# Performance work log

Hardware: AMD Instinct MI355X
Metric: run time of the kernel (lower is better)

## Reference

```python
import jax, jax.numpy as jnp
import numpy as np

DIM = 256      # channel dim
NW = 7         # n_win per side
HEADS = 8
TOPK = 4
KVW = 4        # kv_per_win (ada_avgpool output side)
EPS = 1e-6


def _dwconv(x, w, b):
    # depthwise conv, NHWC, 'SAME' == padding k//2 for odd kernels
    y = jax.lax.conv_general_dilated(
        x, w, (1, 1), 'SAME',
        dimension_numbers=('NHWC', 'HWIO', 'NHWC'),
        feature_group_count=x.shape[-1])
    return y + b


def _ln(x, g, b):
    mu = x.mean(-1, keepdims=True)
    var = ((x - mu) ** 2).mean(-1, keepdims=True)
    return (x - mu) * jax.lax.rsqrt(var + EPS) * g + b


def _bra(x, qkv_w, qkv_b, wo_w, wo_b, lepe_w, lepe_b):
    # BiLevelRoutingAttention, x: (n, H, W, C)
    n, H, W, C = x.shape
    hw, ww = H // NW, W // NW          # window size (8, 8)
    scale = C ** -0.5                   # qk_dim ** -0.5 (BiFormer uses full qk_dim)
    qkv = x @ qkv_w.T + qkv_b           # (n, H, W, 3C)
    # window partition: n (j hw) (i ww) c -> n (j i) hw ww c
    qkv_win = qkv.reshape(n, NW, hw, NW, ww, 3 * C)
    qkv_win = qkv_win.transpose(0, 1, 3, 2, 4, 5).reshape(n, NW * NW, hw, ww, 3 * C)
    q = qkv_win[..., :C]                # (n, p2, hw, ww, C)
    kv = qkv_win[..., C:]               # (n, p2, hw, ww, 2C)
    # --- window-level routing (q/k detached in torch; no fwd effect) ---
    q_win = q.mean((2, 3))              # (n, p2, C)
    k_win = kv[..., :C].mean((2, 3))    # (n, p2, C)
    logits = jnp.einsum('npc,nqc->npq', q_win * scale, k_win)
    _, idx = jax.lax.top_k(logits, TOPK)            # (n, p2, k)
    # --- kv downsample: adaptive avg pool (hw,ww)->(KVW,KVW), exact 2x2 mean here ---
    fh, fw = hw // KVW, ww // KVW
    kv_pix = kv.reshape(n, NW * NW, KVW, fh, KVW, fw, 2 * C).mean((3, 5))
    kv_pix = kv_pix.reshape(n, NW * NW, KVW * KVW, 2 * C)   # (n, p2, w2, 2C)
    # --- gather top-k windows' kv ---
    kv_sel = jax.vmap(lambda t, ix: t[ix])(kv_pix, idx)     # (n, p2, k, w2, 2C)
    cph = C // HEADS
    k_sel = kv_sel[..., :C].reshape(n, NW * NW, TOPK * KVW * KVW, HEADS, cph)
    v_sel = kv_sel[..., C:].reshape(n, NW * NW, TOPK * KVW * KVW, HEADS, cph)
    q_pix = q.reshape(n, NW * NW, hw * ww, HEADS, cph)
    # --- windowed attention over gathered tokens ---
    att = jnp.einsum('npqmc,npsmc->npmqs', q_pix * scale, k_sel)
    att = jax.nn.softmax(att, axis=-1)
    out = jnp.einsum('npmqs,npsmc->npqmc', att, v_sel)
    out = out.reshape(n, NW, NW, hw, ww, C).transpose(0, 1, 3, 2, 4, 5).reshape(n, H, W, C)
    # --- lepe: depthwise 5x5 on v over the full image ---
    v_img = qkv[..., 2 * C:]
    out = out + _dwconv(v_img, lepe_w, lepe_b)
    return out @ wo_w.T + wo_b


def setup_inputs() -> dict:
    key = jax.random.key(0)
    ks = jax.random.split(key, 8)
    C, s = DIM, 0.02
    p = {}
    p['x'] = jax.random.normal(ks[0], (16, C, 56, 56), jnp.float32)
    p['pos_w'] = jax.random.normal(ks[1], (3, 3, 1, C), jnp.float32) * s
    p['pos_b'] = jnp.zeros((C,), jnp.float32)
    p['ln1_g'] = jnp.ones((C,), jnp.float32)
    p['ln1_b'] = jnp.zeros((C,), jnp.float32)
    p['ln2_g'] = jnp.ones((C,), jnp.float32)
    p['ln2_b'] = jnp.zeros((C,), jnp.float32)
    p['qkv_w'] = jax.random.normal(ks[2], (3 * C, C), jnp.float32) * s
    p['qkv_b'] = jnp.zeros((3 * C,), jnp.float32)
    p['wo_w'] = jax.random.normal(ks[3], (C, C), jnp.float32) * s
    p['wo_b'] = jnp.zeros((C,), jnp.float32)
    p['lepe_w'] = jax.random.normal(ks[4], (5, 5, 1, C), jnp.float32) * s
    p['lepe_b'] = jnp.zeros((C,), jnp.float32)
    p['fc1_w'] = jax.random.normal(ks[5], (4 * C, C), jnp.float32) * s
    p['fc1_b'] = jnp.zeros((4 * C,), jnp.float32)
    p['fc2_w'] = jax.random.normal(ks[6], (C, 4 * C), jnp.float32) * s
    p['fc2_b'] = jnp.zeros((C,), jnp.float32)
    return p


def reference(x, pos_w, pos_b, ln1_g, ln1_b, ln2_g, ln2_b, qkv_w, qkv_b,
              wo_w, wo_b, lepe_w, lepe_b, fc1_w, fc1_b, fc2_w, fc2_b):
    xh = x.transpose(0, 2, 3, 1)                       # NCHW -> NHWC
    xh = xh + _dwconv(xh, pos_w, pos_b)                # pos embed (dw 3x3)
    xh = xh + _bra(_ln(xh, ln1_g, ln1_b), qkv_w, qkv_b, wo_w, wo_b, lepe_w, lepe_b)
    h = _ln(xh, ln2_g, ln2_b)
    h = jax.nn.gelu(h @ fc1_w.T + fc1_b, approximate=False)
    xh = xh + (h @ fc2_w.T + fc2_b)
    return xh.transpose(0, 3, 1, 2)                    # NHWC -> NCHW
```

## Files before the change

kernel.cpp:

```cpp
#include <hip/hip_runtime.h>
#include <math.h>

static constexpr int NIMG = 16;
static constexpr int TOK  = NIMG * 56 * 56;
static constexpr size_t TC = (size_t)TOK * 256;
static constexpr int PTOK = 784 * 16;

typedef __bf16 bf16x8 __attribute__((ext_vector_type(8)));
typedef float  f32x4  __attribute__((ext_vector_type(4)));

__device__ inline float bf2f(unsigned short u) {
  unsigned int i = ((unsigned int)u) << 16; float f; __builtin_memcpy(&f, &i, 4); return f;
}
__device__ inline unsigned short f2bf(float f) {
  unsigned int i; __builtin_memcpy(&i, &f, 4);
  unsigned int r = i + 0x7fffu + ((i >> 16) & 1u);
  return (unsigned short)(r >> 16);
}

__global__ __launch_bounds__(256) void nchw2nhwc(const float* __restrict__ x,
                                                 float* __restrict__ y) {
  __shared__ float tile[32][33];
  int nh = blockIdx.z;
  int n = nh / 56, h = nh % 56;
  int c0 = blockIdx.y * 32, w0 = blockIdx.x * 32;
  int tx = threadIdx.x, ty = threadIdx.y;
#pragma unroll
  for (int i = 0; i < 4; i++) {
    int c = c0 + ty + i * 8, w = w0 + tx;
    if (w < 56) tile[ty + i * 8][tx] = x[(((size_t)n * 256 + c) * 56 + h) * 56 + w];
  }
  __syncthreads();
#pragma unroll
  for (int i = 0; i < 4; i++) {
    int w = w0 + ty + i * 8, c = c0 + tx;
    if (w < 56) y[(((size_t)n * 56 + h) * 56 + w) * 256 + c] = tile[tx][ty + i * 8];
  }
}

__global__ __launch_bounds__(256) void nhwc2nchw(const float* __restrict__ y,
                                                 float* __restrict__ o) {
  __shared__ float tile[32][33];
  int nh = blockIdx.z;
  int n = nh / 56, h = nh % 56;
  int w0 = blockIdx.x * 32, c0 = blockIdx.y * 32;
  int tx = threadIdx.x, ty = threadIdx.y;
#pragma unroll
  for (int i = 0; i < 4; i++) {
    int w = w0 + ty + i * 8, c = c0 + tx;
    if (w < 56) tile[ty + i * 8][tx] = y[(((size_t)n * 56 + h) * 56 + w) * 256 + c];
  }
  __syncthreads();
#pragma unroll
  for (int i = 0; i < 4; i++) {
    int c = c0 + ty + i * 8, w = w0 + tx;
    if (w < 56) o[(((size_t)n * 256 + c) * 56 + h) * 56 + w] = tile[tx][ty + i * 8];
  }
}

__global__ __launch_bounds__(256) void posconv_kernel(const float* __restrict__ xt,
                                                      const float* __restrict__ w,
                                                      const float* __restrict__ b,
                                                      float* __restrict__ xh) {
  int t = blockIdx.x * 4 + (threadIdx.x >> 6);
  int lane = threadIdx.x & 63;
  int c = lane * 4;
  int n = t / 3136, rem = t % 3136, h = rem / 56, ww = rem % 56;
  f32x4 acc = *(const f32x4*)&b[c];
  for (int dh = -1; dh <= 1; dh++) {
    int hh = h + dh;
    if ((unsigned)hh >= 56u) continue;
    for (int dw = -1; dw <= 1; dw++) {
      int wc = ww + dw;
      if ((unsigned)wc >= 56u) continue;
      f32x4 xx = *(const f32x4*)&xt[(((size_t)n * 56 + hh) * 56 + wc) * 256 + c];
      f32x4 wv = *(const f32x4*)&w[((dh + 1) * 3 + (dw + 1)) * 256 + c];
      acc += xx * wv;
    }
  }
  f32x4 xv = *(const f32x4*)&xt[(size_t)t * 256 + c];
  *(f32x4*)&xh[(size_t)t * 256 + c] = xv + acc;
}

__global__ __launch_bounds__(256) void lnw_kernel(const float* __restrict__ x,
                                                  const float* __restrict__ g,
                                                  const float* __restrict__ b,
                                                  float* __restrict__ of,
                                                  unsigned short* __restrict__ ob) {
  int t = blockIdx.x * 4 + (threadIdx.x >> 6);
  int lane = threadIdx.x & 63;
  int c = lane * 4;
  f32x4 v = *(const f32x4*)&x[(size_t)t * 256 + c];
  float s = v[0] + v[1] + v[2] + v[3];
#pragma unroll
  for (int m = 1; m < 64; m <<= 1) s += __shfl_xor(s, m);
  float mu = s * (1.f / 256.f);
  f32x4 d = v - mu;
  float ss = d[0] * d[0] + d[1] * d[1] + d[2] * d[2] + d[3] * d[3];
#pragma unroll
  for (int m = 1; m < 64; m <<= 1) ss += __shfl_xor(ss, m);
  float rs = rsqrtf(ss * (1.f / 256.f) + 1e-6f);
  f32x4 gg = *(const f32x4*)&g[c];
  f32x4 bb = *(const f32x4*)&b[c];
  f32x4 y = d * rs * gg + bb;
  if (of) *(f32x4*)&of[(size_t)t * 256 + c] = y;
  if (ob) {
    unsigned short yb[4];
#pragma unroll
    for (int j = 0; j < 4; j++) yb[j] = f2bf(y[j]);
    __builtin_memcpy(ob + (size_t)t * 256 + c, yb, 8);
  }
}

template <bool OUTBF, bool LN2F>
__global__ __launch_bounds__(512, 4) void mgemm2(const unsigned short* __restrict__ A, int lda,
                                                 const unsigned short* __restrict__ B, int ldb,
                                                 const float* __restrict__ bias,
                                                 const float* __restrict__ R,
                                                 void* __restrict__ C_,
                                                 int N, int K, int flags, int gx,
                                                 const float* __restrict__ g2,
                                                 const float* __restrict__ b2,
                                                 unsigned short* __restrict__ ob2) {
  __shared__ unsigned short As[128 * 64];
  __shared__ unsigned short Bs[256 * 64];
  __shared__ float redS[4][128];
  __shared__ float redQ[4][128];
  int tid = threadIdx.x;
  int nwg = gridDim.x, bid = blockIdx.x;
  int q8 = nwg >> 3, r8 = nwg & 7;
  int xcd = bid & 7, pos = bid >> 3;
  int wgid = (xcd < r8 ? xcd * (q8 + 1) : r8 * (q8 + 1) + (xcd - r8) * q8) + pos;
  int m0 = (wgid / gx) * 128;
  int n0 = (wgid % gx) * 256;

  int lane = tid & 63, wid = tid >> 6;
  int wr = (wid >> 2) * 64, wc = (wid & 3) * 64;
  int llo = lane & 15, lhi = lane >> 4;

  f32x4 acc[4][4];
#pragma unroll
  for (int i = 0; i < 4; i++)
#pragma unroll
    for (int j = 0; j < 4; j++) acc[i][j] = (f32x4){0.f, 0.f, 0.f, 0.f};

  for (int k0 = 0; k0 < K; k0 += 64) {
#pragma unroll
    for (int i = 0; i < 2; i++) {
      int qa = tid + 512 * i;
      int row = qa >> 3, col = (qa & 7) ^ (row & 7);
      __builtin_amdgcn_global_load_lds(
          (const __attribute__((address_space(1))) unsigned int*)
              (A + (size_t)(m0 + row) * lda + k0 + col * 8),
          (__attribute__((address_space(3))) unsigned int*)(As + qa * 8), 16, 0, 0);
    }
#pragma unroll
    for (int i = 0; i < 4; i++) {
      int qb = tid + 512 * i;
      int row = qb >> 3, col = (qb & 7) ^ (row & 7);
      __builtin_amdgcn_global_load_lds(
          (const __attribute__((address_space(1))) unsigned int*)
              (B + (size_t)(n0 + row) * ldb + k0 + col * 8),
          (__attribute__((address_space(3))) unsigned int*)(Bs + qb * 8), 16, 0, 0);
    }
    __syncthreads();
#pragma unroll
    for (int ks = 0; ks < 2; ks++) {
      int cchunk = ks * 4 + lhi;
      bf16x8 af[4], bfr[4];
#pragma unroll
      for (int mi = 0; mi < 4; mi++) {
        int r = wr + mi * 16 + llo;
        __builtin_memcpy(&af[mi], As + (size_t)r * 64 + (cchunk ^ (r & 7)) * 8, 16);
      }
#pragma unroll
      for (int nj = 0; nj < 4; nj++) {
        int r = wc + nj * 16 + llo;
        __builtin_memcpy(&bfr[nj], Bs + (size_t)r * 64 + (cchunk ^ (r & 7)) * 8, 16);
      }
#pragma unroll
      for (int mi = 0; mi < 4; mi++)
#pragma unroll
        for (int nj = 0; nj < 4; nj++)
          acc[mi][nj] = __builtin_amdgcn_mfma_f32_16x16x32_bf16(af[mi], bfr[nj],
                                                                acc[mi][nj], 0, 0, 0);
    }
    __syncthreads();
  }

  if constexpr (LN2F) {
    float sr[4][4], qr[4][4];
#pragma unroll
    for (int mi = 0; mi < 4; mi++)
#pragma unroll
      for (int j = 0; j < 4; j++) { sr[mi][j] = 0.f; qr[mi][j] = 0.f; }
#pragma unroll
    for (int mi = 0; mi < 4; mi++)
#pragma unroll
      for (int nj = 0; nj < 4; nj++) {
        int n = wc + nj * 16 + llo;
        float bv = bias[n];
#pragma unroll
        for (int j = 0; j < 4; j++) {
          int m = m0 + wr + mi * 16 + lhi * 4 + j;
          float v = acc[mi][nj][j] + bv + R[(size_t)m * 256 + n];
          acc[mi][nj][j] = v;
          sr[mi][j] += v;
          qr[mi][j] += v * v;
        }
      }
#pragma unroll
    for (int mi = 0; mi < 4; mi++)
#pragma unroll
      for (int j = 0; j < 4; j++)
#pragma unroll
        for (int d = 1; d < 16; d <<= 1) {
          sr[mi][j] += __shfl_xor(sr[mi][j], d);
          qr[mi][j] += __shfl_xor(qr[mi][j], d);
        }
    if (llo == 0) {
#pragma unroll
      for (int mi = 0; mi < 4; mi++)
#pragma unroll
        for (int j = 0; j < 4; j++) {
          int lr = wr + mi * 16 + lhi * 4 + j;
          redS[wid & 3][lr] = sr[mi][j];
          redQ[wid & 3][lr] = qr[mi][j];
        }
    }
    __syncthreads();
#pragma unroll
    for (int mi = 0; mi < 4; mi++)
#pragma unroll
      for (int j = 0; j < 4; j++) {
        int lr = wr + mi * 16 + lhi * 4 + j;
        float S = redS[0][lr] + redS[1][lr] + redS[2][lr] + redS[3][lr];
        float Q = redQ[0][lr] + redQ[1][lr] + redQ[2][lr] + redQ[3][lr];
        float mu = S * (1.f / 256.f);
        float var = Q * (1.f / 256.f) - mu * mu;
        float rs = rsqrtf(var + 1e-6f);
        size_t mrow = (size_t)(m0 + lr) * 256;
#pragma unroll
        for (int nj = 0; nj < 4; nj++) {
          int n = wc + nj * 16 + llo;
          float v = acc[mi][nj][j];
          ((float*)C_)[mrow + n] = v;
          ob2[mrow + n] = f2bf((v - mu) * rs * g2[n] + b2[n]);
        }
      }
  } else {
    int coln = llo, rowg = lhi * 4;
#pragma unroll
    for (int mi = 0; mi < 4; mi++) {
#pragma unroll
      for (int nj = 0; nj < 4; nj++) {
        int n = n0 + wc + nj * 16 + coln;
        float bv = (flags & 8) ? 0.f : bias[n];
#pragma unroll
        for (int j = 0; j < 4; j++) {
          int m = m0 + wr + mi * 16 + rowg + j;
          float v = acc[mi][nj][j] + bv;
          if (flags & 1) v = 0.5f * v * (1.0f + erff(v * 0.70710678118654752f));
          if (flags & 2) v += R[(size_t)m * N + n];
          if (OUTBF) ((unsigned short*)C_)[(size_t)m * N + n] = f2bf(v);
          else       ((float*)C_)[(size_t)m * N + n] = v;
        }
      }
    }
  }
}

__global__ __launch_bounds__(256) void cvt_kernel(const float* __restrict__ s,
                                                  unsigned short* __restrict__ d, int n) {
  int i = blockIdx.x * 256 + threadIdx.x;
  if (i < n) d[i] = f2bf(s[i]);
}

__global__ __launch_bounds__(512) void bqv_kernel(const float* __restrict__ qkv_b,
                                                  float* __restrict__ bqv) {
  int i = threadIdx.x;
  bqv[i] = qkv_b[i < 256 ? i : i + 256];
}

__global__ __launch_bounds__(256) void pool_kernel(const float* __restrict__ x,
                                                   unsigned short* __restrict__ plx,
                                                   float* __restrict__ wmx) {
  int np = blockIdx.x, c = threadIdx.x;
  int n = np / 49, p = np % 49, wr = p / 7, wc = p % 7;
  float tot = 0.f;
  for (int s = 0; s < 16; s++) {
    int i = s >> 2, j = s & 3;
    float a = 0.f;
    for (int di = 0; di < 2; di++)
      for (int dj = 0; dj < 2; dj++) {
        size_t t = ((size_t)n * 56 + wr * 8 + i * 2 + di) * 56 + wc * 8 + j * 2 + dj;
        a += x[t * 256 + c];
      }
    a *= 0.25f;
    plx[((size_t)np * 16 + s) * 256 + c] = f2bf(a);
    tot += a;
  }
  wmx[(size_t)np * 256 + c] = tot * (1.f / 16.f);
}

__global__ __launch_bounds__(256) void winproj_kernel(const float* __restrict__ wmx,
                                                      const float* __restrict__ qkv_w,
                                                      const float* __restrict__ qkv_b,
                                                      float* __restrict__ qkwin) {
  int np = blockIdx.x, t = threadIdx.x;
  __shared__ float xs[256];
  xs[t] = wmx[(size_t)np * 256 + t];
  __syncthreads();
  for (int rep = 0; rep < 2; rep++) {
    int n = t + rep * 256;
    const float* wrow = qkv_w + (size_t)n * 256;
    float s = qkv_b[n];
    for (int c = 0; c < 256; c++) s += xs[c] * wrow[c];
    qkwin[(size_t)np * 512 + n] = s;
  }
}

__global__ __launch_bounds__(64) void topk_kernel(const float* __restrict__ qkwin,
                                                  int* __restrict__ idx) {
  int np = blockIdx.x;
  int n = np / 49;
  int j = threadIdx.x;
  __shared__ float lg[49];
  if (j < 49) {
    const float* qp = qkwin + (size_t)np * 512;
    const float* kp = qkwin + ((size_t)n * 49 + j) * 512 + 256;
    float s = 0.f;
    for (int c = 0; c < 256; c++) s += qp[c] * kp[c];
    lg[j] = s;
  }
  __syncthreads();
  if (j == 0) {
    unsigned long long used = 0ull;
    for (int t = 0; t < 4; t++) {
      float best = -INFINITY;
      int bi = 0;
      for (int q = 0; q < 49; q++)
        if (!((used >> q) & 1ull) && lg[q] > best) { best = lg[q]; bi = q; }
      idx[np * 4 + t] = bi;
      used |= (1ull << bi);
    }
  }
}

__global__ __launch_bounds__(64) void attn_mfma(const unsigned short* __restrict__ qvb,
                                                const unsigned short* __restrict__ kvp,
                                                const int* __restrict__ idx,
                                                unsigned short* __restrict__ out) {
  __shared__ unsigned short Vt[32 * 72];
  __shared__ unsigned short Pl[64 * 72];
  int bid = blockIdx.x;
  int head = bid & 7, np = bid >> 3;
  int n = np / 49, p = np % 49;
  int h0 = (p / 7) * 8, w0 = (p % 7) * 8;
  int lane = threadIdx.x;
  int lhi = lane >> 4, llo = lane & 15;

  int wi4[4];
#pragma unroll
  for (int t = 0; t < 4; t++) wi4[t] = idx[np * 4 + t];

#pragma unroll
  for (int it = 0; it < 4; it++) {
    int cell = lane >> 2;
    int chunk = lane & 3;
    int s = it * 16 + cell;
    const unsigned short* g = kvp + ((size_t)(n * 49 + wi4[it]) * 16 + cell) * 512
                              + 256 + head * 32 + chunk * 8;
    unsigned short vv[8];
    __builtin_memcpy(vv, g, 16);
#pragma unroll
    for (int j = 0; j < 8; j++) Vt[(chunk * 8 + j) * 72 + s] = vv[j];
  }

  bf16x8 qf[4], kf[4];
#pragma unroll
  for (int mi = 0; mi < 4; mi++) {
    int row = mi * 16 + llo;
    int h = h0 + (row >> 3), w = w0 + (row & 7);
    __builtin_memcpy(&qf[mi],
                     qvb + (((size_t)n * 56 + h) * 56 + w) * 512 + head * 32 + lhi * 8, 16);
  }
#pragma unroll
  for (int nj = 0; nj < 4; nj++) {
    __builtin_memcpy(&kf[nj],
                     kvp + ((size_t)(n * 49 + wi4[nj]) * 16 + llo) * 512 + head * 32 + lhi * 8,
                     16);
  }

  f32x4 acc[4][4];
#pragma unroll
  for (int mi = 0; mi < 4; mi++)
#pragma unroll
    for (int nj = 0; nj < 4; nj++) acc[mi][nj] = (f32x4){0.f, 0.f, 0.f, 0.f};
#pragma unroll
  for (int mi = 0; mi < 4; mi++)
#pragma unroll
    for (int nj = 0; nj < 4; nj++)
      acc[mi][nj] = __builtin_amdgcn_mfma_f32_16x16x32_bf16(qf[mi], kf[nj], acc[mi][nj], 0, 0, 0);

#pragma unroll
  for (int mi = 0; mi < 4; mi++)
#pragma unroll
    for (int nj = 0; nj < 4; nj++) acc[mi][nj] *= 0.0625f;
#pragma unroll
  for (int mi = 0; mi < 4; mi++) {
#pragma unroll
    for (int reg = 0; reg < 4; reg++) {
      float m = fmaxf(fmaxf(acc[mi][0][reg], acc[mi][1][reg]),
                      fmaxf(acc[mi][2][reg], acc[mi][3][reg]));
      m = fmaxf(m, __shfl_xor(m, 1));
      m = fmaxf(m, __shfl_xor(m, 2));
      m = fmaxf(m, __shfl_xor(m, 4));
      m = fmaxf(m, __shfl_xor(m, 8));
      float sum = 0.f;
#pragma unroll
      for (int nj = 0; nj < 4; nj++) {
        float e = __expf(acc[mi][nj][reg] - m);
        acc[mi][nj][reg] = e;
        sum += e;
      }
      sum += __shfl_xor(sum, 1);
      sum += __shfl_xor(sum, 2);
      sum += __shfl_xor(sum, 4);
      sum += __shfl_xor(sum, 8);
      float inv = 1.0f / sum;
#pragma unroll
      for (int nj = 0; nj < 4; nj++) acc[mi][nj][reg] *= inv;
    }
  }

#pragma unroll
  for (int mi = 0; mi < 4; mi++)
#pragma unroll
    for (int nj = 0; nj < 4; nj++)
#pragma unroll
      for (int reg = 0; reg < 4; reg++) {
        int row = mi * 16 + lhi * 4 + reg;
        Pl[row * 72 + nj * 16 + llo] = f2bf(acc[mi][nj][reg]);
      }

  f32x4 o[4][2];
#pragma unroll
  for (int mi = 0; mi < 4; mi++)
#pragma unroll
    for (int nc = 0; nc < 2; nc++) o[mi][nc] = (f32x4){0.f, 0.f, 0.f, 0.f};
#pragma unroll
  for (int ks = 0; ks < 2; ks++) {
    bf16x8 pa[4], vb[2];
#pragma unroll
    for (int mi = 0; mi < 4; mi++)
      __builtin_memcpy(&pa[mi], Pl + (mi * 16 + llo) * 72 + ks * 32 + lhi * 8, 16);
#pragma unroll
    for (int nc = 0; nc < 2; nc++)
      __builtin_memcpy(&vb[nc], Vt + (nc * 16 + llo) * 72 + ks * 32 + lhi * 8, 16);
#pragma unroll
    for (int mi = 0; mi < 4; mi++)
#pragma unroll
      for (int nc = 0; nc < 2; nc++)
        o[mi][nc] = __builtin_amdgcn_mfma_f32_16x16x32_bf16(pa[mi], vb[nc], o[mi][nc], 0, 0, 0);
  }

#pragma unroll
  for (int mi = 0; mi < 4; mi++)
#pragma unroll
    for (int nc = 0; nc < 2; nc++)
#pragma unroll
      for (int reg = 0; reg < 4; reg++) {
        int row = mi * 16 + lhi * 4 + reg;
        int h = h0 + (row >> 3), w = w0 + (row & 7);
        out[(((size_t)n * 56 + h) * 56 + w) * 256 + head * 32 + nc * 16 + llo] =
            f2bf(o[mi][nc][reg]);
      }
}

__global__ __launch_bounds__(256) void lepe_kernel(const unsigned short* __restrict__ qvb,
                                                   const float* __restrict__ w,
                                                   const float* __restrict__ b,
                                                   unsigned short* __restrict__ out) {
  int t = blockIdx.x * 8 + (threadIdx.x >> 5);
  int cg = threadIdx.x & 31;
  int c = cg * 8;
  int n = t / 3136, rem = t % 3136, h = rem / 56, ww = rem % 56;
  float acc[8];
#pragma unroll
  for (int j = 0; j < 8; j++) acc[j] = b[c + j];
  for (int dh = -2; dh <= 2; dh++) {
    int hh = h + dh;
    if ((unsigned)hh >= 56u) continue;
    for (int dw = -2; dw <= 2; dw++) {
      int wc = ww + dw;
      if ((unsigned)wc >= 56u) continue;
      unsigned short vv[8];
      __builtin_memcpy(vv, qvb + (((size_t)n * 56 + hh) * 56 + wc) * 512 + 256 + c, 16);
      const float* wp = w + ((dh + 2) * 5 + (dw + 2)) * 256 + c;
#pragma unroll
      for (int j = 0; j < 8; j++) acc[j] += bf2f(vv[j]) * wp[j];
    }
  }
  size_t o = (size_t)t * 256 + c;
  unsigned short ov[8];
  __builtin_memcpy(ov, out + o, 16);
#pragma unroll
  for (int j = 0; j < 8; j++) ov[j] = f2bf(bf2f(ov[j]) + acc[j]);
  __builtin_memcpy(out + o, ov, 16);
}

extern "C" void kernel_launch(void* const* d_in, const int* in_sizes, int n_in,
                              void* d_out, int out_size, void* d_ws, size_t ws_size,
                              hipStream_t stream) {
  const float* x      = (const float*)d_in[0];
  const float* pos_w  = (const float*)d_in[1];
  const float* pos_b  = (const float*)d_in[2];
  const float* ln1_g  = (const float*)d_in[3];
  const float* ln1_b  = (const float*)d_in[4];
  const float* ln2_g  = (const float*)d_in[5];
  const float* ln2_b  = (const float*)d_in[6];
  const float* qkv_w  = (const float*)d_in[7];
  const float* qkv_b  = (const float*)d_in[8];
  const float* wo_w   = (const float*)d_in[9];
  const float* wo_b   = (const float*)d_in[10];
  const float* lepe_w = (const float*)d_in[11];
  const float* lepe_b = (const float*)d_in[12];
  const float* fc1_w  = (const float*)d_in[13];
  const float* fc1_b  = (const float*)d_in[14];
  const float* fc2_w  = (const float*)d_in[15];
  const float* fc2_b  = (const float*)d_in[16];

  float*          xt   = (float*)d_out;
  float*          lnf  = (float*)d_out;
  unsigned short* qvb  = (unsigned short*)d_out;
  unsigned short* hbuf = (unsigned short*)d_out;

  float*          r2   = (float*)d_ws;
  float*          wmx  = r2 + TC;
  float*          qkw  = wmx + (size_t)784 * 256;
  float*          bqv  = qkw + (size_t)784 * 512;
  unsigned short* lnb  = (unsigned short*)(bqv + 512);
  unsigned short* aob  = lnb;
  unsigned short* ln2b = lnb;
  unsigned short* plx  = lnb + TC;
  unsigned short* kvp  = plx + (size_t)PTOK * 256;
  unsigned short* wqv  = kvp + (size_t)PTOK * 512;
  unsigned short* wkv  = wqv + (size_t)512 * 256;
  unsigned short* wwo  = wkv + (size_t)512 * 256;
  unsigned short* wfc1 = wwo + (size_t)256 * 256;
  unsigned short* wfc2 = wfc1 + (size_t)1024 * 256;
  int*            idx  = (int*)(wfc2 + (size_t)256 * 1024);

  cvt_kernel<<<(65536 + 255) / 256, 256, 0, stream>>>(qkv_w, wqv, 65536);
  cvt_kernel<<<(65536 + 255) / 256, 256, 0, stream>>>(qkv_w + (size_t)512 * 256, wqv + 65536, 65536);
  cvt_kernel<<<(131072 + 255) / 256, 256, 0, stream>>>(qkv_w + (size_t)256 * 256, wkv, 131072);
  cvt_kernel<<<(65536 + 255) / 256, 256, 0, stream>>>(wo_w, wwo, 65536);
  cvt_kernel<<<(262144 + 255) / 256, 256, 0, stream>>>(fc1_w, wfc1, 262144);
  cvt_kernel<<<(262144 + 255) / 256, 256, 0, stream>>>(fc2_w, wfc2, 262144);
  bqv_kernel<<<1, 512, 0, stream>>>(qkv_b, bqv);

  dim3 tb(32, 8);
  nchw2nhwc<<<dim3(2, 8, NIMG * 56), tb, 0, stream>>>(x, xt);
  posconv_kernel<<<TOK / 4, 256, 0, stream>>>(xt, pos_w, pos_b, r2);
  lnw_kernel<<<TOK / 4, 256, 0, stream>>>(r2, ln1_g, ln1_b, lnf, lnb);
  pool_kernel<<<784, 256, 0, stream>>>(lnf, plx, wmx);
  mgemm2<true, false><<<784, 512, 0, stream>>>(lnb, 256, wqv, 256, bqv, nullptr,
                                               qvb, 512, 256, 0, 2,
                                               nullptr, nullptr, nullptr);
  mgemm2<true, false><<<196, 512, 0, stream>>>(plx, 256, wkv, 256, qkv_b + 256, nullptr,
                                               kvp, 512, 256, 0, 2,
                                               nullptr, nullptr, nullptr);
  winproj_kernel<<<784, 256, 0, stream>>>(wmx, qkv_w, qkv_b, qkw);
  topk_kernel<<<784, 64, 0, stream>>>(qkw, idx);
  attn_mfma<<<6272, 64, 0, stream>>>(qvb, kvp, idx, aob);
  lepe_kernel<<<TOK / 8, 256, 0, stream>>>(qvb, lepe_w, lepe_b, aob);
  mgemm2<false, true><<<392, 512, 0, stream>>>(aob, 256, wwo, 256, wo_b, r2,
                                               r2, 256, 256, 2, 1,
                                               ln2_g, ln2_b, ln2b);
  mgemm2<true, false><<<784, 512, 0, stream>>>(ln2b, 256, wfc1, 256, fc1_b, nullptr,
                                               hbuf, 512, 256, 1, 2,
                                               nullptr, nullptr, nullptr);
  mgemm2<false, false><<<392, 512, 0, stream>>>(hbuf, 512, wfc2, 1024, fc2_b, r2,
                                                r2, 256, 512, 2, 1,
                                                nullptr, nullptr, nullptr);
  mgemm2<true, false><<<784, 512, 0, stream>>>(ln2b, 256, wfc1 + (size_t)512 * 256, 256,
                                               fc1_b + 512, nullptr,
                                               hbuf, 512, 256, 1, 2,
                                               nullptr, nullptr, nullptr);
  mgemm2<false, false><<<392, 512, 0, stream>>>(hbuf, 512, wfc2 + 512, 1024, fc2_b, r2,
                                                r2, 256, 512, 2 | 8, 1,
                                                nullptr, nullptr, nullptr);
  nhwc2nchw<<<dim3(2, 8, NIMG * 56), tb, 0, stream>>>(r2, (float*)d_out);
}
```

Before: 527.8 us.

## Vectorize layout transposes and pooling, remap block order in stencil kernels

Rewrites the NCHW/NHWC transpose kernels to load and store 16-byte float4 vectors through a padded shared tile, using a flat 256-thread block. The pooling kernel now covers four windows per block, each on its own wavefront, with float4 loads and 8-byte bf16 stores. The positional and LePE depthwise conv kernels remap block IDs in a round-robin by 8 so that neighbouring token ranges are spread across blocks, likely aimed at the XCD chiplets. The goal is fewer memory transactions and better cache locality in bandwidth-bound helper kernels. The risk is LDS bank conflicts in the strided tile reads.

New measurement: 508.1 us. -3.7%, faster.

```diff
diff --git a/kernel.cpp b/kernel.cpp
--- a/kernel.cpp
+++ b/kernel.cpp
@@ -20,41 +20,57 @@
 
 __global__ __launch_bounds__(256) void nchw2nhwc(const float* __restrict__ x,
                                                  float* __restrict__ y) {
-  __shared__ float tile[32][33];
+  __shared__ float T[32][37];
   int nh = blockIdx.z;
   int n = nh / 56, h = nh % 56;
   int c0 = blockIdx.y * 32, w0 = blockIdx.x * 32;
-  int tx = threadIdx.x, ty = threadIdx.y;
-#pragma unroll
-  for (int i = 0; i < 4; i++) {
-    int c = c0 + ty + i * 8, w = w0 + tx;
-    if (w < 56) tile[ty + i * 8][tx] = x[(((size_t)n * 256 + c) * 56 + h) * 56 + w];
+  int tid = threadIdx.x;
+  int wlim = 56 - w0; if (wlim > 32) wlim = 32;
+  {
+    int ci = tid >> 3, w = (tid & 7) * 4;
+    if (w < wlim) {
+      f32x4 v = *(const f32x4*)&x[(((size_t)n * 256 + c0 + ci) * 56 + h) * 56 + w0 + w];
+#pragma unroll
+      for (int j = 0; j < 4; j++) T[ci][w + j] = v[j];
+    }
   }
   __syncthreads();
-#pragma unroll
-  for (int i = 0; i < 4; i++) {
-    int w = w0 + ty + i * 8, c = c0 + tx;
-    if (w < 56) y[(((size_t)n * 56 + h) * 56 + w) * 256 + c] = tile[tx][ty + i * 8];
+  {
+    int wi = tid >> 3, cq = tid & 7;
+    if (wi < wlim) {
+      f32x4 o;
+#pragma unroll
+      for (int k = 0; k < 4; k++) o[k] = T[cq * 4 + k][wi];
+      *(f32x4*)&y[(((size_t)n * 56 + h) * 56 + w0 + wi) * 256 + c0 + cq * 4] = o;
+    }
   }
 }
 
 __global__ __launch_bounds__(256) void nhwc2nchw(const float* __restrict__ y,
                                                  float* __restrict__ o) {
-  __shared__ float tile[32][33];
+  __shared__ float T[32][37];
   int nh = blockIdx.z;
   int n = nh / 56, h = nh % 56;
   int w0 = blockIdx.x * 32, c0 = blockIdx.y * 32;
-  int tx = threadIdx.x, ty = threadIdx.y;
-#pragma unroll
-  for (int i = 0; i < 4; i++) {
-    int w = w0 + ty + i * 8, c = c0 + tx;
-    if (w < 56) tile[ty + i * 8][tx] = y[(((size_t)n * 56 + h) * 56 + w) * 256 + c];
+  int tid = threadIdx.x;
+  int wlim = 56 - w0; if (wlim > 32) wlim = 32;
+  {
+    int wi = tid >> 3, cq = tid & 7;
+    if (wi < wlim) {
+      f32x4 v = *(const f32x4*)&y[(((size_t)n * 56 + h) * 56 + w0 + wi) * 256 + c0 + cq * 4];
+#pragma unroll
+      for (int k = 0; k < 4; k++) T[wi][cq * 4 + k] = v[k];
+    }
   }
   __syncthreads();
-#pragma unroll
-  for (int i = 0; i < 4; i++) {
-    int c = c0 + ty + i * 8, w = w0 + tx;
-    if (w < 56) o[(((size_t)n * 256 + c) * 56 + h) * 56 + w] = tile[tx][ty + i * 8];
+  {
+    int ci = tid >> 3, w = (tid & 7) * 4;
+    if (w < wlim) {
+      f32x4 ov;
+#pragma unroll
+      for (int j = 0; j < 4; j++) ov[j] = T[w + j][ci];
+      *(f32x4*)&o[(((size_t)n * 256 + c0 + ci) * 56 + h) * 56 + w0 + w] = ov;
+    }
   }
 }
 
@@ -62,7 +78,9 @@
                                                       const float* __restrict__ w,
                                                       const float* __restrict__ b,
                                                       float* __restrict__ xh) {
-  int t = blockIdx.x * 4 + (threadIdx.x >> 6);
+  int bid = blockIdx.x;
+  int wgid = (bid & 7) * 1568 + (bid >> 3);
+  int t = wgid * 4 + (threadIdx.x >> 6);
   int lane = threadIdx.x & 63;
   int c = lane * 4;
   int n = t / 3136, rem = t % 3136, h = rem / 56, ww = rem % 56;
@@ -285,22 +303,27 @@
 __global__ __launch_bounds__(256) void pool_kernel(const float* __restrict__ x,
                                                    unsigned short* __restrict__ plx,
                                                    float* __restrict__ wmx) {
-  int np = blockIdx.x, c = threadIdx.x;
+  int np = blockIdx.x * 4 + (threadIdx.x >> 6);
+  int lane = threadIdx.x & 63;
+  int c = lane * 4;
   int n = np / 49, p = np % 49, wr = p / 7, wc = p % 7;
-  float tot = 0.f;
+  f32x4 tot = (f32x4){0.f, 0.f, 0.f, 0.f};
   for (int s = 0; s < 16; s++) {
     int i = s >> 2, j = s & 3;
-    float a = 0.f;
+    f32x4 a = (f32x4){0.f, 0.f, 0.f, 0.f};
     for (int di = 0; di < 2; di++)
       for (int dj = 0; dj < 2; dj++) {
         size_t t = ((size_t)n * 56 + wr * 8 + i * 2 + di) * 56 + wc * 8 + j * 2 + dj;
-        a += x[t * 256 + c];
+        a += *(const f32x4*)&x[t * 256 + c];
       }
     a *= 0.25f;
-    plx[((size_t)np * 16 + s) * 256 + c] = f2bf(a);
+    unsigned short ab[4];
+#pragma unroll
+    for (int k = 0; k < 4; k++) ab[k] = f2bf(a[k]);
+    __builtin_memcpy(plx + ((size_t)np * 16 + s) * 256 + c, ab, 8);
     tot += a;
   }
-  wmx[(size_t)np * 256 + c] = tot * (1.f / 16.f);
+  *(f32x4*)&wmx[(size_t)np * 256 + c] = tot * (1.f / 16.f);
 }
 
 __global__ __launch_bounds__(256) void winproj_kernel(const float* __restrict__ wmx,
@@ -482,7 +505,9 @@
                                                    const float* __restrict__ w,
                                                    const float* __restrict__ b,
                                                    unsigned short* __restrict__ out) {
-  int t = blockIdx.x * 8 + (threadIdx.x >> 5);
+  int bid = blockIdx.x;
+  int wgid = (bid & 7) * 784 + (bid >> 3);
+  int t = wgid * 8 + (threadIdx.x >> 5);
   int cg = threadIdx.x & 31;
   int c = cg * 8;
   int n = t / 3136, rem = t % 3136, h = rem / 56, ww = rem % 56;
@@ -561,10 +586,10 @@
   bqv_kernel<<<1, 512, 0, stream>>>(qkv_b, bqv);
 
   dim3 tb(32, 8);
-  nchw2nhwc<<<dim3(2, 8, NIMG * 56), tb, 0, stream>>>(x, xt);
+  nchw2nhwc<<<dim3(2, 8, NIMG * 56), 256, 0, stream>>>(x, xt);
   posconv_kernel<<<TOK / 4, 256, 0, stream>>>(xt, pos_w, pos_b, r2);
   lnw_kernel<<<TOK / 4, 256, 0, stream>>>(r2, ln1_g, ln1_b, lnf, lnb);
-  pool_kernel<<<784, 256, 0, stream>>>(lnf, plx, wmx);
+  pool_kernel<<<196, 256, 0, stream>>>(lnf, plx, wmx);
   mgemm2<true, false><<<784, 512, 0, stream>>>(lnb, 256, wqv, 256, bqv, nullptr,
                                                qvb, 512, 256, 0, 2,
                                                nullptr, nullptr, nullptr);
@@ -591,5 +616,5 @@
   mgemm2<false, false><<<392, 512, 0, stream>>>(hbuf, 512, wfc2 + 512, 1024, fc2_b, r2,
                                                 r2, 256, 512, 2 | 8, 1,
                                                 nullptr, nullptr, nullptr);
-  nhwc2nchw<<<dim3(2, 8, NIMG * 56), tb, 0, stream>>>(r2, (float*)d_out);
-}
+  nhwc2nchw<<<dim3(2, 8, NIMG * 56), 256, 0, stream>>>(r2, (float*)d_out);
+}
```
